# Kernel tuning notes

Hardware: AMD Instinct MI355X
Metric: run time of the kernel (lower is better)

Reference implementation:

```python
import math
import jax, jax.numpy as jnp
import numpy as np

C, B, T, D = 8, 4, 8192, 64
MAX_LEN = 8192
_DELTA = math.log2(MAX_LEN) / max(C - 1, 1)
# lam_c = 1 - 2^{-(c*delta)}; lam_0 == 0 (memoryless channel)
LAMBDAS = jnp.array([1.0 - 2.0 ** (-(c * _DELTA)) for c in range(C)], dtype=jnp.float32)


def setup_inputs() -> dict:
    key = jax.random.key(0)
    k0, k1, k2 = jax.random.split(key, 3)
    return {
        "channels": jax.random.normal(k0, (C, B, T, D), dtype=jnp.float32),
        "gw_fwd": jax.random.normal(k1, (C, D, D), dtype=jnp.float32) * 0.02,
        "gb_fwd": jnp.ones((C, D), dtype=jnp.float32),
        "gw_bwd": jax.random.normal(k2, (C, D, D), dtype=jnp.float32) * 0.02,
        "gb_bwd": jnp.ones((C, D), dtype=jnp.float32),
    }


def _fixed_decay_scan(lam, v):
    """h_t = lam * h_{t-1} + v_t over axis=1 (time); v: [B,T,D], lam scalar.
    For lam==0 this reduces to identity, matching the torch fast path."""
    a = jnp.full_like(v, lam)

    def combine(x, y):
        a1, b1 = x
        a2, b2 = y
        return (a1 * a2, a2 * b1 + b2)

    return jax.lax.associative_scan(combine, (a, v), axis=1)[1]


def _run_direction(channels, W, b):
    # torch Linear: y = x @ W.T + b, W is (out,in) -> einsum 'cbtd,ced->cbte'
    g = jax.nn.sigmoid(jnp.einsum('cbtd,ced->cbte', channels, W) + b[:, None, None, :])
    gated = g * channels
    return jax.vmap(_fixed_decay_scan)(LAMBDAS, gated)  # [C,B,T,D]


def reference(channels, gw_fwd, gb_fwd, gw_bwd, gb_bwd):
    fwd = _run_direction(channels, gw_fwd, gb_fwd)
    rev = channels[:, :, ::-1, :]
    bwd = _run_direction(rev, gw_bwd, gb_bwd)[:, :, ::-1, :]
    return fwd, bwd
```

## Files before the change

kernel.cpp:

```cpp
#include <hip/hip_runtime.h>
#include <cmath>
#include <cstdint>

typedef __attribute__((ext_vector_type(8))) short short8;
typedef __attribute__((ext_vector_type(4))) float f32x4;
typedef __attribute__((ext_vector_type(2))) unsigned int u32x2;

struct Lams { float v[8]; };

#define NC 8
#define NB 4
#define NT 8192
#define ND 64
#define CL 256
#define NCHUNK 32
#define NKK 16
#define NBLK (2 * NC * NB * NKK)
#define NSLOT (2 * NC * NB * NCHUNK)
#define NWAVE 8
#define LDH 72

__device__ __forceinline__ uint32_t pk2(float lo, float hi) {
    uint32_t r;
    asm("v_cvt_pk_bf16_f32 %0, %1, %2" : "=v"(r) : "v"(lo), "v"(hi));
    return r;
}

__device__ __forceinline__ float bf2f(unsigned short s) {
    return __builtin_bit_cast(float, (uint32_t)s << 16);
}
__device__ __forceinline__ float bflo(uint32_t u) { return bf2f((unsigned short)(u & 0xFFFFu)); }
__device__ __forceinline__ float bfhi(uint32_t u) { return bf2f((unsigned short)(u >> 16)); }

__global__ __launch_bounds__(512, 4) void k1_fused(
    const float* __restrict__ x, const float* __restrict__ Wf,
    const float* __restrict__ bf, const float* __restrict__ Wb,
    const float* __restrict__ bb, float* __restrict__ out,
    int* __restrict__ flags, float* __restrict__ evals, Lams lams)
{
    __shared__ unsigned short xbuf[CL * LDH];
    __shared__ float ends_lds[NWAVE][ND];
    __shared__ float hprev_lds[ND];

    const int tid  = threadIdx.x;
    const int lane = tid & 63;
    const int w    = tid >> 6;

    int idx = blockIdx.x;
    const int kk  = idx & (NKK - 1); idx >>= 4;
    const int b   = idx & (NB - 1);  idx >>= 2;
    const int c   = idx & (NC - 1);  idx >>= 3;
    const int dir = idx;

    const float lam = lams.v[c];
    const float* W    = (dir ? Wb : Wf) + c * ND * ND;
    const float* bias = (dir ? bb : bf) + c * ND;
    const float* xb   = x + (size_t)(c * NB + b) * NT * ND;
    float* ob = out + (size_t)dir * (size_t)(NC*NB*NT*ND)
                    + (size_t)(c * NB + b) * NT * ND;
    const int seqbase = (int)(blockIdx.x >> 4) * NCHUNK;

    const int er = lane & 15;
    const int ks = lane >> 4;
    const int r0 = w * 32;

    short8 bfrag[4][2];
    #pragma unroll
    for (int et = 0; et < 4; ++et) {
        const float* wr = W + (et*16 + er) * ND + ks * 8;
        #pragma unroll
        for (int kq = 0; kq < 2; ++kq) {
            f32x4 lo = *reinterpret_cast<const f32x4*>(wr + kq*32);
            f32x4 hi = *reinterpret_cast<const f32x4*>(wr + kq*32 + 4);
            union { short8 s8; uint32_t u[4]; } t;
            t.u[0] = pk2(lo[0], lo[1]); t.u[1] = pk2(lo[2], lo[3]);
            t.u[2] = pk2(hi[0], hi[1]); t.u[3] = pk2(hi[2], hi[3]);
            bfrag[et][kq] = t.s8;
        }
    }
    float bias_r[4];
    #pragma unroll
    for (int et = 0; et < 4; ++et) bias_r[et] = bias[et*16 + er];

    float lam32 = lam*lam; lam32*=lam32; lam32*=lam32; lam32*=lam32; lam32*=lam32;

    #pragma unroll 1
    for (int pass = 0; pass < 2; ++pass) {
        const int g   = kk + NKK * pass;
        const int tr0 = g * CL;

        {
            const int sr = lane >> 4;
            const int sc = (lane & 15) * 4;
            if (dir == 0) {
                const float* p = xb + (size_t)(tr0 + r0 + sr) * ND + sc;
                #pragma unroll
                for (int q = 0; q < 8; ++q) {
                    f32x4 v = *reinterpret_cast<const f32x4*>(p + (size_t)q * 4 * ND);
                    u32x2 u = { pk2(v[0], v[1]), pk2(v[2], v[3]) };
                    *reinterpret_cast<u32x2*>(&xbuf[(r0 + q*4 + sr) * LDH + sc]) = u;
                }
            } else {
                const float* p = xb + (size_t)(NT-1 - (tr0 + r0 + sr)) * ND + sc;
                #pragma unroll
                for (int q = 0; q < 8; ++q) {
                    f32x4 v = *reinterpret_cast<const f32x4*>(p - (size_t)q * 4 * ND);
                    u32x2 u = { pk2(v[0], v[1]), pk2(v[2], v[3]) };
                    *reinterpret_cast<u32x2*>(&xbuf[(r0 + q*4 + sr) * LDH + sc]) = u;
                }
            }
        }

        #pragma unroll
        for (int u = 0; u < 2; ++u) {
            const int rl0 = r0 + u*16;
            short8 afrag[2];
            afrag[0] = *reinterpret_cast<const short8*>(&xbuf[(rl0 + er) * LDH + ks * 8]);
            afrag[1] = *reinterpret_cast<const short8*>(&xbuf[(rl0 + er) * LDH + 32 + ks * 8]);
            #pragma unroll
            for (int et = 0; et < 4; ++et) {
                f32x4 acc = {0.f, 0.f, 0.f, 0.f};
                acc = __builtin_amdgcn_mfma_f32_16x16x32_bf16(afrag[0], bfrag[et][0], acc, 0,0,0);
                acc = __builtin_amdgcn_mfma_f32_16x16x32_bf16(afrag[1], bfrag[et][1], acc, 0,0,0);
                const int col = et*16 + er;
                float gated[4];
                #pragma unroll
                for (int r = 0; r < 4; ++r) {
                    const int rl = rl0 + ks*4 + r;
                    float z  = acc[r] + bias_r[et];
                    float gg = __builtin_amdgcn_rcpf(1.0f + __expf(-z));
                    float xv = bf2f(xbuf[rl * LDH + col]);
                    gated[r] = gg * xv;
                }
                uint32_t p01 = pk2(gated[0], gated[1]);
                uint32_t p23 = pk2(gated[2], gated[3]);
                xbuf[(rl0 + ks*4 + 0) * LDH + col] = (unsigned short)(p01 & 0xFFFF);
                xbuf[(rl0 + ks*4 + 1) * LDH + col] = (unsigned short)(p01 >> 16);
                xbuf[(rl0 + ks*4 + 2) * LDH + col] = (unsigned short)(p23 & 0xFFFF);
                xbuf[(rl0 + ks*4 + 3) * LDH + col] = (unsigned short)(p23 >> 16);
            }
        }

        {
            float h = 0.f;
            #pragma unroll
            for (int i = 0; i < 32; ++i) {
                const int a = (r0 + i) * LDH + lane;
                float v = bf2f(xbuf[a]);
                h = fmaf(h, lam, v);
                xbuf[a] = (unsigned short)(pk2(h, h) & 0xFFFF);
            }
            ends_lds[w][lane] = h;
        }
        __syncthreads();

        if (w == NWAVE - 1) {
            float carryW = 0.f;
            #pragma unroll
            for (int j = 0; j < NWAVE - 1; ++j)
                carryW = fmaf(carryW, lam32, ends_lds[j][lane]);
            float E = fmaf(carryW, lam32, ends_lds[NWAVE-1][lane]);

            float Hprev = 0.f;
            if (c != 0) {
                const int slot = seqbase + g;
                __hip_atomic_store(&evals[(size_t)slot * ND + lane], E,
                                   __ATOMIC_RELAXED, __HIP_MEMORY_SCOPE_AGENT);
                asm volatile("s_waitcnt vmcnt(0)" ::: "memory");
                if (lane == 0)
                    __hip_atomic_store(&flags[slot], 1, __ATOMIC_RELAXED,
                                       __HIP_MEMORY_SCOPE_AGENT);
                if (g != 0) {
                    if (lane < g) {
                        while (__hip_atomic_load(&flags[seqbase + lane], __ATOMIC_RELAXED,
                                                 __HIP_MEMORY_SCOPE_AGENT) == 0)
                            __builtin_amdgcn_s_sleep(2);
                    }
                    asm volatile("" ::: "memory");
                    const float* eb = evals + (size_t)seqbase * ND;
                    float l1 = lam32*lam32; l1 *= l1; l1 *= l1;
                    float l4 = l1 * l1; l4 *= l4;
                    float P = 0.f;
                    int j = 0;
                    const int rem = g & 3;
                    for (; j < rem; ++j)
                        P = fmaf(P, l1, eb[(size_t)j * ND + lane]);
                    for (; j < g; j += 4) {
                        float e0 = eb[(size_t)(j+0) * ND + lane];
                        float e1 = eb[(size_t)(j+1) * ND + lane];
                        float e2 = eb[(size_t)(j+2) * ND + lane];
                        float e3 = eb[(size_t)(j+3) * ND + lane];
                        float t = fmaf(fmaf(fmaf(e0, l1, e1), l1, e2), l1, e3);
                        P = fmaf(P, l4, t);
                    }
                    Hprev = P;
                }
            }
            hprev_lds[lane] = Hprev;
        }
        __syncthreads();

        {
            const int sr = lane >> 4;
            const int dg = lane & 15;
            float carry4[4];
            #pragma unroll
            for (int j2 = 0; j2 < 4; ++j2) {
                const int d = dg*4 + j2;
                float cy = 0.f, pw = 1.f;
                for (int j = 0; j < w; ++j) {
                    cy = fmaf(cy, lam32, ends_lds[j][d]);
                    pw *= lam32;
                }
                carry4[j2] = fmaf(pw, hprev_lds[d], cy);
            }
            const float lam2 = lam * lam, lam4 = lam2 * lam2;
            float f = lam;
            for (int j = 0; j < sr; ++j) f *= lam;
            if (dir == 0) {
                float* p = ob + (size_t)(tr0 + r0 + sr) * ND + dg*4;
                #pragma unroll
                for (int q = 0; q < 8; ++q) {
                    u32x2 hv = *reinterpret_cast<const u32x2*>(
                        &xbuf[(r0 + q*4 + sr) * LDH + dg*4]);
                    f32x4 o;
                    o[0] = fmaf(f, carry4[0], bflo(hv[0]));
                    o[1] = fmaf(f, carry4[1], bfhi(hv[0]));
                    o[2] = fmaf(f, carry4[2], bflo(hv[1]));
                    o[3] = fmaf(f, carry4[3], bfhi(hv[1]));
                    *reinterpret_cast<f32x4*>(p + (size_t)q * 4 * ND) = o;
                    f *= lam4;
                }
            } else {
                float* p = ob + (size_t)(NT-1 - (tr0 + r0 + sr)) * ND + dg*4;
                #pragma unroll
                for (int q = 0; q < 8; ++q) {
                    u32x2 hv = *reinterpret_cast<const u32x2*>(
                        &xbuf[(r0 + q*4 + sr) * LDH + dg*4]);
                    f32x4 o;
                    o[0] = fmaf(f, carry4[0], bflo(hv[0]));
                    o[1] = fmaf(f, carry4[1], bfhi(hv[0]));
                    o[2] = fmaf(f, carry4[2], bflo(hv[1]));
                    o[3] = fmaf(f, carry4[3], bfhi(hv[1]));
                    *reinterpret_cast<f32x4*>(p - (size_t)q * 4 * ND) = o;
                    f *= lam4;
                }
            }
        }
        __syncthreads();
    }
}

extern "C" void kernel_launch(void* const* d_in, const int* in_sizes, int n_in,
                              void* d_out, int out_size, void* d_ws, size_t ws_size,
                              hipStream_t stream)
{
    const float* x  = (const float*)d_in[0];
    const float* Wf = (const float*)d_in[1];
    const float* bf = (const float*)d_in[2];
    const float* Wb = (const float*)d_in[3];
    const float* bb = (const float*)d_in[4];
    float* out = (float*)d_out;

    int*   flags = (int*)d_ws;
    float* evals = (float*)((char*)d_ws + 16384);

    Lams lams;
    const double delta = 13.0 / 7.0;
    for (int c = 0; c < 8; ++c)
        lams.v[c] = (float)(1.0 - pow(2.0, -(double)c * delta));

    hipMemsetAsync(flags, 0, NSLOT * 4, stream);

    dim3 grid(NBLK);
    k1_fused<<<grid, 512, 0, stream>>>(x, Wf, bf, Wb, bb, out, flags, evals, lams);
}
```

Measured before the change: 70.33 us.

## Halve chunk size, run four passes with double-buffered LDS prefetch

Chunk length drops from 256 to 128 rows, so each block handles four passes instead of two and holds two LDS buffers. While the last wave resolves the cross-chunk carry (flag wait plus evals reduction), the other waves prefetch and convert the next chunk's input into the spare buffer. The intent is to hide global load latency and the decoupled look-back stall behind each other. In exchange there are more look-back slots and passes per block and more LDS use, which may reduce occupancy. The flags and evals arrays must be sized for the doubled slot count.

Result: slower. 86.55 us (+23.1%).

```diff
diff --git a/kernel.cpp b/kernel.cpp
--- a/kernel.cpp
+++ b/kernel.cpp
@@ -12,12 +12,14 @@
 #define NB 4
 #define NT 8192
 #define ND 64
-#define CL 256
-#define NCHUNK 32
+#define CL 128
+#define NP 4
+#define NCHUNK 64
 #define NKK 16
 #define NBLK (2 * NC * NB * NKK)
 #define NSLOT (2 * NC * NB * NCHUNK)
 #define NWAVE 8
+#define WR 16
 #define LDH 72
 
 __device__ __forceinline__ uint32_t pk2(float lo, float hi) {
@@ -38,7 +40,7 @@
     const float* __restrict__ bb, float* __restrict__ out,
     int* __restrict__ flags, float* __restrict__ evals, Lams lams)
 {
-    __shared__ unsigned short xbuf[CL * LDH];
+    __shared__ unsigned short xbuf[2][CL * LDH];
     __shared__ float ends_lds[NWAVE][ND];
     __shared__ float hprev_lds[ND];
 
@@ -62,7 +64,30 @@
 
     const int er = lane & 15;
     const int ks = lane >> 4;
-    const int r0 = w * 32;
+    const int r0 = w * WR;
+
+    auto STAGE = [&](int B, int gc, int rb) {
+        const int sr = lane >> 4;
+        const int sc = (lane & 15) * 4;
+        const int tr = gc * CL + rb + sr;
+        if (dir == 0) {
+            const float* p = xb + (size_t)tr * ND + sc;
+            #pragma unroll
+            for (int q = 0; q < 4; ++q) {
+                f32x4 v = *reinterpret_cast<const f32x4*>(p + (size_t)q * 4 * ND);
+                u32x2 u = { pk2(v[0], v[1]), pk2(v[2], v[3]) };
+                *reinterpret_cast<u32x2*>(&xbuf[B][(rb + q*4 + sr) * LDH + sc]) = u;
+            }
+        } else {
+            const float* p = xb + (size_t)(NT-1 - tr) * ND + sc;
+            #pragma unroll
+            for (int q = 0; q < 4; ++q) {
+                f32x4 v = *reinterpret_cast<const f32x4*>(p - (size_t)q * 4 * ND);
+                u32x2 u = { pk2(v[0], v[1]), pk2(v[2], v[3]) };
+                *reinterpret_cast<u32x2*>(&xbuf[B][(rb + q*4 + sr) * LDH + sc]) = u;
+            }
+        }
+    };
 
     short8 bfrag[4][2];
     #pragma unroll
@@ -82,41 +107,20 @@
     #pragma unroll
     for (int et = 0; et < 4; ++et) bias_r[et] = bias[et*16 + er];
 
-    float lam32 = lam*lam; lam32*=lam32; lam32*=lam32; lam32*=lam32; lam32*=lam32;
+    float lam16 = lam*lam; lam16*=lam16; lam16*=lam16; lam16*=lam16;
+
+    STAGE(0, kk, r0);
 
     #pragma unroll 1
-    for (int pass = 0; pass < 2; ++pass) {
-        const int g   = kk + NKK * pass;
+    for (int p = 0; p < NP; ++p) {
+        const int P   = p & 1;
+        const int g   = kk + NKK * p;
         const int tr0 = g * CL;
 
         {
-            const int sr = lane >> 4;
-            const int sc = (lane & 15) * 4;
-            if (dir == 0) {
-                const float* p = xb + (size_t)(tr0 + r0 + sr) * ND + sc;
-                #pragma unroll
-                for (int q = 0; q < 8; ++q) {
-                    f32x4 v = *reinterpret_cast<const f32x4*>(p + (size_t)q * 4 * ND);
-                    u32x2 u = { pk2(v[0], v[1]), pk2(v[2], v[3]) };
-                    *reinterpret_cast<u32x2*>(&xbuf[(r0 + q*4 + sr) * LDH + sc]) = u;
-                }
-            } else {
-                const float* p = xb + (size_t)(NT-1 - (tr0 + r0 + sr)) * ND + sc;
-                #pragma unroll
-                for (int q = 0; q < 8; ++q) {
-                    f32x4 v = *reinterpret_cast<const f32x4*>(p - (size_t)q * 4 * ND);
-                    u32x2 u = { pk2(v[0], v[1]), pk2(v[2], v[3]) };
-                    *reinterpret_cast<u32x2*>(&xbuf[(r0 + q*4 + sr) * LDH + sc]) = u;
-                }
-            }
-        }
-
-        #pragma unroll
-        for (int u = 0; u < 2; ++u) {
-            const int rl0 = r0 + u*16;
             short8 afrag[2];
-            afrag[0] = *reinterpret_cast<const short8*>(&xbuf[(rl0 + er) * LDH + ks * 8]);
-            afrag[1] = *reinterpret_cast<const short8*>(&xbuf[(rl0 + er) * LDH + 32 + ks * 8]);
+            afrag[0] = *reinterpret_cast<const short8*>(&xbuf[P][(r0 + er) * LDH + ks * 8]);
+            afrag[1] = *reinterpret_cast<const short8*>(&xbuf[P][(r0 + er) * LDH + 32 + ks * 8]);
             #pragma unroll
             for (int et = 0; et < 4; ++et) {
                 f32x4 acc = {0.f, 0.f, 0.f, 0.f};
@@ -126,31 +130,33 @@
                 float gated[4];
                 #pragma unroll
                 for (int r = 0; r < 4; ++r) {
-                    const int rl = rl0 + ks*4 + r;
+                    const int rl = r0 + ks*4 + r;
                     float z  = acc[r] + bias_r[et];
                     float gg = __builtin_amdgcn_rcpf(1.0f + __expf(-z));
-                    float xv = bf2f(xbuf[rl * LDH + col]);
+                    float xv = bf2f(xbuf[P][rl * LDH + col]);
                     gated[r] = gg * xv;
                 }
                 uint32_t p01 = pk2(gated[0], gated[1]);
                 uint32_t p23 = pk2(gated[2], gated[3]);
-                xbuf[(rl0 + ks*4 + 0) * LDH + col] = (unsigned short)(p01 & 0xFFFF);
-                xbuf[(rl0 + ks*4 + 1) * LDH + col] = (unsigned short)(p01 >> 16);
-                xbuf[(rl0 + ks*4 + 2) * LDH + col] = (unsigned short)(p23 & 0xFFFF);
-                xbuf[(rl0 + ks*4 + 3) * LDH + col] = (unsigned short)(p23 >> 16);
-            }
-        }
-
+                xbuf[P][(r0 + ks*4 + 0) * LDH + col] = (unsigned short)(p01 & 0xFFFF);
+                xbuf[P][(r0 + ks*4 + 1) * LDH + col] = (unsigned short)(p01 >> 16);
+                xbuf[P][(r0 + ks*4 + 2) * LDH + col] = (unsigned short)(p23 & 0xFFFF);
+                xbuf[P][(r0 + ks*4 + 3) * LDH + col] = (unsigned short)(p23 >> 16);
+            }
+        }
+
+        float hend;
         {
             float h = 0.f;
             #pragma unroll
-            for (int i = 0; i < 32; ++i) {
+            for (int i = 0; i < WR; ++i) {
                 const int a = (r0 + i) * LDH + lane;
-                float v = bf2f(xbuf[a]);
+                float v = bf2f(xbuf[P][a]);
                 h = fmaf(h, lam, v);
-                xbuf[a] = (unsigned short)(pk2(h, h) & 0xFFFF);
+                xbuf[P][a] = (unsigned short)(pk2(h, h) & 0xFFFF);
             }
             ends_lds[w][lane] = h;
+            hend = h;
         }
         __syncthreads();
 
@@ -158,8 +164,8 @@
             float carryW = 0.f;
             #pragma unroll
             for (int j = 0; j < NWAVE - 1; ++j)
-                carryW = fmaf(carryW, lam32, ends_lds[j][lane]);
-            float E = fmaf(carryW, lam32, ends_lds[NWAVE-1][lane]);
+                carryW = fmaf(carryW, lam16, ends_lds[j][lane]);
+            float E = fmaf(carryW, lam16, hend);
 
             float Hprev = 0.f;
             if (c != 0) {
@@ -178,25 +184,29 @@
                     }
                     asm volatile("" ::: "memory");
                     const float* eb = evals + (size_t)seqbase * ND;
-                    float l1 = lam32*lam32; l1 *= l1; l1 *= l1;
+                    float l1 = lam16 * lam16; l1 *= l1; l1 *= l1;
                     float l4 = l1 * l1; l4 *= l4;
-                    float P = 0.f;
+                    float P2 = 0.f;
                     int j = 0;
                     const int rem = g & 3;
                     for (; j < rem; ++j)
-                        P = fmaf(P, l1, eb[(size_t)j * ND + lane]);
+                        P2 = fmaf(P2, l1, eb[(size_t)j * ND + lane]);
                     for (; j < g; j += 4) {
                         float e0 = eb[(size_t)(j+0) * ND + lane];
                         float e1 = eb[(size_t)(j+1) * ND + lane];
                         float e2 = eb[(size_t)(j+2) * ND + lane];
                         float e3 = eb[(size_t)(j+3) * ND + lane];
                         float t = fmaf(fmaf(fmaf(e0, l1, e1), l1, e2), l1, e3);
-                        P = fmaf(P, l4, t);
+                        P2 = fmaf(P2, l4, t);
                     }
-                    Hprev = P;
+                    Hprev = P2;
                 }
             }
             hprev_lds[lane] = Hprev;
+        } else if (p + 1 < NP) {
+            STAGE(P ^ 1, kk + NKK * (p + 1), r0);
+            if (w == 0)
+                STAGE(P ^ 1, kk + NKK * (p + 1), 7 * WR);
         }
         __syncthreads();
 
@@ -209,8 +219,8 @@
                 const int d = dg*4 + j2;
                 float cy = 0.f, pw = 1.f;
                 for (int j = 0; j < w; ++j) {
-                    cy = fmaf(cy, lam32, ends_lds[j][d]);
-                    pw *= lam32;
+                    cy = fmaf(cy, lam16, ends_lds[j][d]);
+                    pw *= lam16;
                 }
                 carry4[j2] = fmaf(pw, hprev_lds[d], cy);
             }
@@ -218,31 +228,31 @@
             float f = lam;
             for (int j = 0; j < sr; ++j) f *= lam;
             if (dir == 0) {
-                float* p = ob + (size_t)(tr0 + r0 + sr) * ND + dg*4;
+                float* pp = ob + (size_t)(tr0 + r0 + sr) * ND + dg*4;
                 #pragma unroll
-                for (int q = 0; q < 8; ++q) {
+                for (int q = 0; q < 4; ++q) {
                     u32x2 hv = *reinterpret_cast<const u32x2*>(
-                        &xbuf[(r0 + q*4 + sr) * LDH + dg*4]);
+                        &xbuf[P][(r0 + q*4 + sr) * LDH + dg*4]);
                     f32x4 o;
                     o[0] = fmaf(f, carry4[0], bflo(hv[0]));
                     o[1] = fmaf(f, carry4[1], bfhi(hv[0]));
                     o[2] = fmaf(f, carry4[2], bflo(hv[1]));
                     o[3] = fmaf(f, carry4[3], bfhi(hv[1]));
-                    *reinterpret_cast<f32x4*>(p + (size_t)q * 4 * ND) = o;
+                    *reinterpret_cast<f32x4*>(pp + (size_t)q * 4 * ND) = o;
                     f *= lam4;
                 }
             } else {
-                float* p = ob + (size_t)(NT-1 - (tr0 + r0 + sr)) * ND + dg*4;
+                float* pp = ob + (size_t)(NT-1 - (tr0 + r0 + sr)) * ND + dg*4;
                 #pragma unroll
-                for (int q = 0; q < 8; ++q) {
+                for (int q = 0; q < 4; ++q) {
                     u32x2 hv = *reinterpret_cast<const u32x2*>(
-                        &xbuf[(r0 + q*4 + sr) * LDH + dg*4]);
+                        &xbuf[P][(r0 + q*4 + sr) * LDH + dg*4]);
                     f32x4 o;
                     o[0] = fmaf(f, carry4[0], bflo(hv[0]));
                     o[1] = fmaf(f, carry4[1], bfhi(hv[0]));
                     o[2] = fmaf(f, carry4[2], bflo(hv[1]));
                     o[3] = fmaf(f, carry4[3], bfhi(hv[1]));
-                    *reinterpret_cast<f32x4*>(p - (size_t)q * 4 * ND) = o;
+                    *reinterpret_cast<f32x4*>(pp - (size_t)q * 4 * ND) = o;
                     f *= lam4;
                 }
             }
```
